# Kernel tuning notes

Measured on AMD Instinct MI355X. Metric: run time of the kernel, lower is better.

## Reference

```python
import jax, jax.numpy as jnp
import numpy as np

B, S, DIM = 2, 2048, 1024
H = 16
HD = DIM // H  # 64
SCALE = HD ** -0.5


def setup_inputs() -> dict:
    key = jax.random.key(0)
    k1, k2, k3 = jax.random.split(key, 3)
    x = jax.random.normal(k1, (B, S, DIM), dtype=jnp.float32)
    # Linear weights scaled ~1/sqrt(fan_in) like torch default init
    Wqkv = jax.random.normal(k2, (DIM, 3 * DIM), dtype=jnp.float32) * (DIM ** -0.5)
    Wproj = jax.random.normal(k3, (DIM, DIM), dtype=jnp.float32) * (DIM ** -0.5)
    return {"x": x, "Wqkv": Wqkv, "Wproj": Wproj}


def reference(x, Wqkv, Wproj):
    Bsz, Slen, dim = x.shape
    qkv = x @ Wqkv  # (B, S, 3*dim)
    qkv = qkv.reshape(Bsz, Slen, 3, H, HD)
    q, k, v = qkv[:, :, 0], qkv[:, :, 1], qkv[:, :, 2]  # each (B, S, H, HD)
    # softmax attention (chunking in the original is memory-only; math identical)
    scores = jnp.einsum("bshd,bthd->bhst", q, k) * SCALE  # (B, H, S, S)
    attn = jax.nn.softmax(scores, axis=-1)
    out = jnp.einsum("bhst,bthd->bshd", attn, v)  # (B, S, H, HD)
    out = out.reshape(Bsz, Slen, dim)
    return out @ Wproj
```

## Files before the change

### kernel.cpp

```cpp
#include <hip/hip_runtime.h>
#include <stdint.h>

typedef unsigned short u16;
typedef __attribute__((ext_vector_type(8))) short bf16x8;
typedef __attribute__((ext_vector_type(4))) float f32x4;

#define BATCH 2
#define SEQ 2048
#define NH 16
#define HDIM 64
#define DMODEL 1024
#define MTOT (BATCH * SEQ)
#define QKV_N (3 * DMODEL)
#define ATT_SCALE 0.125f
#define L2E 1.44269504088896340736f
#define C2 (ATT_SCALE * L2E)

__device__ __forceinline__ u16 f2b(float f) {
    uint32_t x = __builtin_bit_cast(uint32_t, f);
    uint32_t r = (x + 0x7fffu + ((x >> 16) & 1u)) >> 16;
    return (u16)r;
}

__device__ __forceinline__ uint32_t cvt_pk(float lo, float hi) {
    uint32_t r;
    asm("v_cvt_pk_bf16_f32 %0, %1, %2" : "=v"(r) : "v"(lo), "v"(hi));
    return r;
}

__device__ __forceinline__ void gl_lds16(const void* g, void* l) {
    __builtin_amdgcn_global_load_lds(
        (const __attribute__((address_space(1))) void*)g,
        (__attribute__((address_space(3))) void*)l, 16, 0, 0);
}

__global__ __launch_bounds__(256) void k_cvt(const float* __restrict__ in,
                                             u16* __restrict__ out, int n8) {
    int i = blockIdx.x * blockDim.x + threadIdx.x;
    if (i >= n8) return;
    const float4* p = (const float4*)in + (size_t)i * 2;
    float4 a = p[0], b = p[1];
    union { uint32_t w[4]; uint4 v; } u;
    u.w[0] = cvt_pk(a.x, a.y);
    u.w[1] = cvt_pk(a.z, a.w);
    u.w[2] = cvt_pk(b.x, b.y);
    u.w[3] = cvt_pk(b.z, b.w);
    *(uint4*)(out + (size_t)i * 8) = u.v;
}

__global__ __launch_bounds__(256) void k_wtrans(const float* __restrict__ W,
                                                u16* __restrict__ WT,
                                                int rows, int cols) {
    __shared__ float tile[64][65];
    const int c0 = blockIdx.x * 64, r0 = blockIdx.y * 64;
    const int tx = threadIdx.x & 63, ty = threadIdx.x >> 6;
#pragma unroll
    for (int i = 0; i < 16; ++i) {
        int r = i * 4 + ty;
        tile[r][tx] = W[(size_t)(r0 + r) * cols + c0 + tx];
    }
    __syncthreads();
#pragma unroll
    for (int i = 0; i < 16; ++i) {
        int c = i * 4 + ty;
        WT[(size_t)(c0 + c) * rows + r0 + tx] = f2b(tile[tx][c]);
    }
}

template <bool F32OUT>
__global__ __launch_bounds__(256) void k_gemm_bt(const u16* __restrict__ A,
                                                 const u16* __restrict__ BT,
                                                 void* __restrict__ C,
                                                 int M, int N, int K) {
    __shared__ __align__(16) u16 As[128 * 64];
    __shared__ __align__(16) u16 Bs[128 * 64];
    const int tid = threadIdx.x;
    const int wid = tid >> 6, lane = tid & 63;
    const int r = lane & 15, g = lane >> 4;
    const int m0 = blockIdx.y * 128, n0 = blockIdx.x * 128;
    const int wm = (wid >> 1) * 64, wn = (wid & 1) * 64;
    const int srow = lane >> 3, scol = (lane & 7) * 8;
    f32x4 acc[4][4] = {};
    for (int k0 = 0; k0 < K; k0 += 64) {
#pragma unroll
        for (int i = 0; i < 4; ++i) {
            const int li = wid * 4 + i;
            gl_lds16(A + (size_t)(m0 + li * 8 + srow) * K + k0 + scol, &As[li * 512]);
            gl_lds16(BT + (size_t)(n0 + li * 8 + srow) * K + k0 + scol, &Bs[li * 512]);
        }
        __syncthreads();
#pragma unroll
        for (int kk = 0; kk < 2; ++kk) {
            bf16x8 af[4], bfr[4];
#pragma unroll
            for (int mi = 0; mi < 4; ++mi)
                af[mi] = *(const bf16x8*)&As[(wm + mi * 16 + r) * 64 + kk * 32 + g * 8];
#pragma unroll
            for (int ni = 0; ni < 4; ++ni)
                bfr[ni] = *(const bf16x8*)&Bs[(wn + ni * 16 + r) * 64 + kk * 32 + g * 8];
#pragma unroll
            for (int mi = 0; mi < 4; ++mi)
#pragma unroll
                for (int ni = 0; ni < 4; ++ni)
                    acc[mi][ni] = __builtin_amdgcn_mfma_f32_16x16x32_bf16(
                        bfr[ni], af[mi], acc[mi][ni], 0, 0, 0);
        }
        __syncthreads();
    }
#pragma unroll
    for (int mi = 0; mi < 4; ++mi)
#pragma unroll
        for (int ni = 0; ni < 4; ++ni) {
            const int row = m0 + wm + mi * 16 + r;
            const int col = n0 + wn + ni * 16 + g * 4;
            if (F32OUT) {
                float4 vv;
                vv.x = acc[mi][ni][0]; vv.y = acc[mi][ni][1];
                vv.z = acc[mi][ni][2]; vv.w = acc[mi][ni][3];
                *(float4*)&((float*)C)[(size_t)row * N + col] = vv;
            } else {
                union { uint32_t w[2]; ushort4 v; } o;
                o.w[0] = cvt_pk(acc[mi][ni][0], acc[mi][ni][1]);
                o.w[1] = cvt_pk(acc[mi][ni][2], acc[mi][ni][3]);
                *(ushort4*)&((u16*)C)[(size_t)row * N + col] = o.v;
            }
        }
}

__global__ __launch_bounds__(256) void k_vtrans(const u16* __restrict__ qkv,
                                                u16* __restrict__ Vt) {
    __shared__ u16 tile[64][65];
    const int bh = blockIdx.y;
    const int b = bh >> 4, h = bh & 15;
    const int s0 = blockIdx.x * 64;
    const int tx = threadIdx.x & 63, ty = threadIdx.x >> 6;
#pragma unroll
    for (int i = 0; i < 16; ++i) {
        int s = i * 4 + ty;
        tile[s][tx] = qkv[(size_t)(b * SEQ + s0 + s) * QKV_N + 2 * DMODEL + h * HDIM + tx];
    }
    __syncthreads();
#pragma unroll
    for (int i = 0; i < 16; ++i) {
        int hd = i * 4 + ty;
        Vt[((size_t)bh * HDIM + hd) * SEQ + s0 + tx] = tile[tx][hd];
    }
}

__global__ __launch_bounds__(256) void k_attn(const u16* __restrict__ qkv,
                                              const u16* __restrict__ Vt,
                                              u16* __restrict__ O) {
    __shared__ __align__(16) u16 Ks[2][4096];
    __shared__ __align__(16) u16 Vs[2][4096];
    const int bh = blockIdx.y;
    const int b = bh >> 4, h = bh & 15;
    const int q0 = blockIdx.x * 64;
    const int tid = threadIdx.x, wid = tid >> 6, lane = tid & 63;
    const int r = lane & 15, g = lane >> 4;

    const size_t qbase = (size_t)(b * SEQ + q0 + wid * 16 + r) * QKV_N + h * HDIM;
    const bf16x8 qf0 = *(const bf16x8*)&qkv[qbase + g * 8];
    const bf16x8 qf1 = *(const bf16x8*)&qkv[qbase + 32 + g * 8];

    float mL = -1e30f, lsum = 0.f;
    f32x4 oacc[4] = {};

    const int kc0 = wid * 2;

#define STAGE(BUF, SK0)                                                          \
    {                                                                            \
        _Pragma("unroll") for (int i = 0; i < 2; ++i) {                          \
            const int kc = kc0 + i;                                              \
            const int ksrow = (kc >> 2) * 32 + g * 8 + (kc & 1) * 4 + ((lane >> 2) & 3); \
            const int kscol = ((kc >> 1) & 1) * 32 + (lane & 3) * 8;             \
            gl_lds16(&qkv[(size_t)(b * SEQ + (SK0) + ksrow) * QKV_N + DMODEL +   \
                          h * HDIM + kscol],                                     \
                     &Ks[BUF][kc * 512]);                                        \
            const int vhd = (kc & 3) * 16 + r;                                   \
            const int vsc = (kc >> 2) * 32 + g * 8;                              \
            gl_lds16(&Vt[((size_t)bh * HDIM + vhd) * SEQ + (SK0) + vsc],         \
                     &Vs[BUF][kc * 512]);                                        \
        }                                                                        \
    }

    STAGE(0, 0);
    asm volatile("s_waitcnt vmcnt(0)");
    __syncthreads();

    for (int t = 0; t < SEQ / 64; ++t) {
        const int cur = t & 1;
        if (t < SEQ / 64 - 1) STAGE(cur ^ 1, (t + 1) * 64);

        f32x4 sacc[4] = {};
        __builtin_amdgcn_s_setprio(1);
#pragma unroll
        for (int nf = 0; nf < 4; ++nf) {
            const int kbase = (nf & 1) * 2048 + (nf >> 1) * 512 +
                              (r >> 2) * 128 + (r & 3) * 32 + g * 8;
            bf16x8 kf0 = *(const bf16x8*)&Ks[cur][kbase];
            bf16x8 kf1 = *(const bf16x8*)&Ks[cur][kbase + 1024];
            sacc[nf] = __builtin_amdgcn_mfma_f32_16x16x32_bf16(kf0, qf0, sacc[nf], 0, 0, 0);
            sacc[nf] = __builtin_amdgcn_mfma_f32_16x16x32_bf16(kf1, qf1, sacc[nf], 0, 0, 0);
        }
        __builtin_amdgcn_s_setprio(0);

        float mt = fmaxf(fmaxf(sacc[0][0], sacc[0][1]), fmaxf(sacc[0][2], sacc[0][3]));
#pragma unroll
        for (int nf = 1; nf < 4; ++nf)
            mt = fmaxf(mt, fmaxf(fmaxf(sacc[nf][0], sacc[nf][1]),
                                 fmaxf(sacc[nf][2], sacc[nf][3])));
        mt = fmaxf(mt, __shfl_xor(mt, 16, 64));
        mt = fmaxf(mt, __shfl_xor(mt, 32, 64));
        const float pm = mt * C2;
        if (!__all(pm - mL <= 8.f)) {
            const float mNew = fmaxf(mL, pm);
            const float al = exp2f(mL - mNew);
            mL = mNew;
            lsum *= al;
#pragma unroll
            for (int ht = 0; ht < 4; ++ht)
#pragma unroll
                for (int e = 0; e < 4; ++e) oacc[ht][e] *= al;
        }
        float p[4][4];
#pragma unroll
        for (int nf = 0; nf < 4; ++nf)
#pragma unroll
            for (int e = 0; e < 4; ++e) {
                p[nf][e] = exp2f(sacc[nf][e] * C2 - mL);
                lsum += p[nf][e];
            }

        union { uint32_t w[4]; bf16x8 v; } upf0, upf1;
        upf0.w[0] = cvt_pk(p[0][0], p[0][1]);
        upf0.w[1] = cvt_pk(p[0][2], p[0][3]);
        upf0.w[2] = cvt_pk(p[2][0], p[2][1]);
        upf0.w[3] = cvt_pk(p[2][2], p[2][3]);
        upf1.w[0] = cvt_pk(p[1][0], p[1][1]);
        upf1.w[1] = cvt_pk(p[1][2], p[1][3]);
        upf1.w[2] = cvt_pk(p[3][0], p[3][1]);
        upf1.w[3] = cvt_pk(p[3][2], p[3][3]);

        __builtin_amdgcn_s_setprio(1);
#pragma unroll
        for (int ht = 0; ht < 4; ++ht) {
            bf16x8 vf0 = *(const bf16x8*)&Vs[cur][ht * 512 + g * 128 + r * 8];
            bf16x8 vf1 = *(const bf16x8*)&Vs[cur][(4 + ht) * 512 + g * 128 + r * 8];
            oacc[ht] = __builtin_amdgcn_mfma_f32_16x16x32_bf16(vf0, upf0.v, oacc[ht], 0, 0, 0);
            oacc[ht] = __builtin_amdgcn_mfma_f32_16x16x32_bf16(vf1, upf1.v, oacc[ht], 0, 0, 0);
        }
        __builtin_amdgcn_s_setprio(0);

        asm volatile("s_waitcnt vmcnt(0)");
        __syncthreads();
    }
#undef STAGE

    lsum += __shfl_xor(lsum, 16, 64);
    lsum += __shfl_xor(lsum, 32, 64);
    const float inv = 1.0f / lsum;
    const size_t obase = (size_t)(b * SEQ + q0 + wid * 16 + r) * DMODEL + h * HDIM;
#pragma unroll
    for (int ht = 0; ht < 4; ++ht) {
        union { uint32_t w[2]; ushort4 v; } o;
        o.w[0] = cvt_pk(oacc[ht][0] * inv, oacc[ht][1] * inv);
        o.w[1] = cvt_pk(oacc[ht][2] * inv, oacc[ht][3] * inv);
        *(ushort4*)&O[obase + ht * 16 + g * 4] = o.v;
    }
}

extern "C" void kernel_launch(void* const* d_in, const int* in_sizes, int n_in,
                              void* d_out, int out_size, void* d_ws, size_t ws_size,
                              hipStream_t stream) {
    const float* x = (const float*)d_in[0];
    const float* Wqkv = (const float*)d_in[1];
    const float* Wproj = (const float*)d_in[2];
    float* out = (float*)d_out;

    u16* xb = (u16*)d_ws;
    u16* WqkvT = xb + (size_t)MTOT * DMODEL;
    u16* WprojT = WqkvT + (size_t)QKV_N * DMODEL;
    u16* qkv = WprojT + (size_t)DMODEL * DMODEL;
    u16* Vt = qkv + (size_t)MTOT * QKV_N;
    u16* Ob = Vt + (size_t)BATCH * NH * HDIM * SEQ;

    k_cvt<<<dim3((MTOT * DMODEL / 8) / 256), 256, 0, stream>>>(x, xb, MTOT * DMODEL / 8);
    k_wtrans<<<dim3(QKV_N / 64, DMODEL / 64), 256, 0, stream>>>(Wqkv, WqkvT, DMODEL, QKV_N);
    k_wtrans<<<dim3(DMODEL / 64, DMODEL / 64), 256, 0, stream>>>(Wproj, WprojT, DMODEL, DMODEL);
    k_gemm_bt<false><<<dim3(QKV_N / 128, MTOT / 128), 256, 0, stream>>>(
        xb, WqkvT, (void*)qkv, MTOT, QKV_N, DMODEL);
    k_vtrans<<<dim3(SEQ / 64, BATCH * NH), 256, 0, stream>>>(qkv, Vt);
    k_attn<<<dim3(SEQ / 64, BATCH * NH), 256, 0, stream>>>(qkv, Vt, Ob);
    k_gemm_bt<true><<<dim3(DMODEL / 128, MTOT / 128), 256, 0, stream>>>(
        Ob, WprojT, (void*)out, MTOT, DMODEL, DMODEL);
}
```

Before: 243.0 us.

## Add 256x256 8-wave ping-pong QKV GEMM and defer softmax max reduction

Swaps the QKV projection GEMM to a new 256x256-tile, 512-thread kernel. It double-buffers A/B tiles in 128KB of dynamic LDS, interleaves LDS reads, global prefetches and MFMA phases with explicit barriers and priority hints, and uses partial vmcnt waits. The aim is to raise data reuse and overlap memory traffic with compute compared with the 128x128 GEMM. The attention kernel also skips the cross-lane max shuffles unless a rescale is needed. The large tile gives only 12x16 blocks, which may underfill the CUs, and the manual barrier scheduling is fragile.

After: 230.3 us. 1.06x faster.

```diff
diff --git a/kernel.cpp b/kernel.cpp
--- a/kernel.cpp
+++ b/kernel.cpp
@@ -15,6 +15,8 @@
 #define ATT_SCALE 0.125f
 #define L2E 1.44269504088896340736f
 #define C2 (ATT_SCALE * L2E)
+
+#define BAR() asm volatile("s_barrier" ::: "memory")
 
 __device__ __forceinline__ u16 f2b(float f) {
     uint32_t x = __builtin_bit_cast(uint32_t, f);
@@ -65,6 +67,131 @@
         int c = i * 4 + ty;
         WT[(size_t)(c0 + c) * rows + r0 + tx] = f2b(tile[tx][c]);
     }
+}
+
+__global__ __launch_bounds__(512, 2) void k_gemm_qkv8(const u16* __restrict__ A,
+                                                      const u16* __restrict__ BT,
+                                                      u16* __restrict__ C) {
+    extern __shared__ __align__(16) u16 lds[];
+    const int tid = threadIdx.x, wid = tid >> 6, lane = tid & 63;
+    const int r = lane & 15, g = lane >> 4;
+    const int wr = wid >> 2, wc = wid & 3;
+    const int m0 = blockIdx.y * 256, n0 = blockIdx.x * 256;
+    const int K = DMODEL;
+
+    auto STG = [&](int kt2, int rg) {
+        const int isB = rg >> 1, half = rg & 1;
+        const u16* src = isB ? BT : A;
+        const int rowb = (isB ? n0 : m0) + half * 128 + wid * 16 + (lane >> 2);
+        const u16* s = src + (size_t)rowb * K + kt2 * 64 + (lane & 3) * 8;
+        const int dst = (kt2 & 1) * 32768 + isB * 16384 + half * 8192 +
+                        wid * 1024 + lane * 8;
+        gl_lds16(s, &lds[dst]);
+        gl_lds16(s + 32, &lds[dst + 512]);
+    };
+
+    f32x4 acc[8][4] = {};
+    bf16x8 a[4][2], b[4][2];
+    const int aB = wr * 8192 + r * 32 + g * 8;
+    const int bB = 16384 + (wc >> 1) * 8192 + (wc & 1) * 4096 + r * 32 + g * 8;
+
+#pragma unroll
+    for (int t2 = 0; t2 < 2; ++t2)
+#pragma unroll
+        for (int rg = 0; rg < 4; ++rg) STG(t2, rg);
+    asm volatile("s_waitcnt vmcnt(0)" ::: "memory");
+    __syncthreads();
+
+    for (int kt = 0; kt < 16; ++kt) {
+        const int sb = (kt & 1) * 32768;
+#pragma unroll
+        for (int mi = 0; mi < 4; ++mi)
+#pragma unroll
+            for (int kk = 0; kk < 2; ++kk)
+                a[mi][kk] = *(const bf16x8*)&lds[sb + aB + (mi * 2 + kk) * 512];
+#pragma unroll
+        for (int ni = 0; ni < 2; ++ni)
+#pragma unroll
+            for (int kk = 0; kk < 2; ++kk)
+                b[ni][kk] = *(const bf16x8*)&lds[sb + bB + (ni * 2 + kk) * 512];
+        BAR();
+        __builtin_amdgcn_s_setprio(1);
+#pragma unroll
+        for (int mi = 0; mi < 4; ++mi)
+#pragma unroll
+            for (int ni = 0; ni < 2; ++ni)
+#pragma unroll
+                for (int kk = 0; kk < 2; ++kk)
+                    acc[mi][ni] = __builtin_amdgcn_mfma_f32_16x16x32_bf16(
+                        b[ni][kk], a[mi][kk], acc[mi][ni], 0, 0, 0);
+        __builtin_amdgcn_s_setprio(0);
+        BAR();
+#pragma unroll
+        for (int ni = 2; ni < 4; ++ni)
+#pragma unroll
+            for (int kk = 0; kk < 2; ++kk)
+                b[ni][kk] = *(const bf16x8*)&lds[sb + bB + (ni * 2 + kk) * 512];
+        BAR();
+        __builtin_amdgcn_s_setprio(1);
+#pragma unroll
+        for (int mi = 0; mi < 4; ++mi)
+#pragma unroll
+            for (int ni = 2; ni < 4; ++ni)
+#pragma unroll
+                for (int kk = 0; kk < 2; ++kk)
+                    acc[mi][ni] = __builtin_amdgcn_mfma_f32_16x16x32_bf16(
+                        b[ni][kk], a[mi][kk], acc[mi][ni], 0, 0, 0);
+        __builtin_amdgcn_s_setprio(0);
+        BAR();
+#pragma unroll
+        for (int mi = 0; mi < 4; ++mi)
+#pragma unroll
+            for (int kk = 0; kk < 2; ++kk)
+                a[mi][kk] = *(const bf16x8*)&lds[sb + aB + ((4 + mi) * 2 + kk) * 512];
+        if (kt < 14) { STG(kt + 2, 2); STG(kt + 2, 3); }
+        BAR();
+        __builtin_amdgcn_s_setprio(1);
+#pragma unroll
+        for (int mi = 0; mi < 4; ++mi)
+#pragma unroll
+            for (int ni = 2; ni < 4; ++ni)
+#pragma unroll
+                for (int kk = 0; kk < 2; ++kk)
+                    acc[4 + mi][ni] = __builtin_amdgcn_mfma_f32_16x16x32_bf16(
+                        b[ni][kk], a[mi][kk], acc[4 + mi][ni], 0, 0, 0);
+        __builtin_amdgcn_s_setprio(0);
+        BAR();
+        if (kt < 14) { STG(kt + 2, 0); STG(kt + 2, 1); }
+        BAR();
+        __builtin_amdgcn_s_setprio(1);
+#pragma unroll
+        for (int mi = 0; mi < 4; ++mi)
+#pragma unroll
+            for (int ni = 0; ni < 2; ++ni)
+#pragma unroll
+                for (int kk = 0; kk < 2; ++kk)
+                    acc[4 + mi][ni] = __builtin_amdgcn_mfma_f32_16x16x32_bf16(
+                        b[ni][kk], a[mi][kk], acc[4 + mi][ni], 0, 0, 0);
+        __builtin_amdgcn_s_setprio(0);
+        if (kt < 14) {
+            asm volatile("s_waitcnt vmcnt(8)" ::: "memory");
+        } else if (kt == 14) {
+            asm volatile("s_waitcnt vmcnt(0)" ::: "memory");
+        }
+        BAR();
+    }
+
+#pragma unroll
+    for (int mi = 0; mi < 8; ++mi)
+#pragma unroll
+        for (int ni = 0; ni < 4; ++ni) {
+            const int row = m0 + wr * 128 + mi * 16 + r;
+            const int col = n0 + wc * 64 + ni * 16 + g * 4;
+            union { uint32_t w[2]; ushort4 v; } o;
+            o.w[0] = cvt_pk(acc[mi][ni][0], acc[mi][ni][1]);
+            o.w[1] = cvt_pk(acc[mi][ni][2], acc[mi][ni][3]);
+            *(ushort4*)&C[(size_t)row * QKV_N + col] = o.v;
+        }
 }
 
 template <bool F32OUT>
@@ -164,7 +291,6 @@
 
     float mL = -1e30f, lsum = 0.f;
     f32x4 oacc[4] = {};
-
     const int kc0 = wid * 2;
 
 #define STAGE(BUF, SK0)                                                          \
@@ -204,16 +330,16 @@
         }
         __builtin_amdgcn_s_setprio(0);
 
-        float mt = fmaxf(fmaxf(sacc[0][0], sacc[0][1]), fmaxf(sacc[0][2], sacc[0][3]));
-#pragma unroll
-        for (int nf = 1; nf < 4; ++nf)
-            mt = fmaxf(mt, fmaxf(fmaxf(sacc[nf][0], sacc[nf][1]),
-                                 fmaxf(sacc[nf][2], sacc[nf][3])));
-        mt = fmaxf(mt, __shfl_xor(mt, 16, 64));
-        mt = fmaxf(mt, __shfl_xor(mt, 32, 64));
-        const float pm = mt * C2;
-        if (!__all(pm - mL <= 8.f)) {
-            const float mNew = fmaxf(mL, pm);
+        float m0a = fmaxf(fmaxf(sacc[0][0], sacc[0][1]), fmaxf(sacc[0][2], sacc[0][3]));
+        float m1a = fmaxf(fmaxf(sacc[1][0], sacc[1][1]), fmaxf(sacc[1][2], sacc[1][3]));
+        float m2a = fmaxf(fmaxf(sacc[2][0], sacc[2][1]), fmaxf(sacc[2][2], sacc[2][3]));
+        float m3a = fmaxf(fmaxf(sacc[3][0], sacc[3][1]), fmaxf(sacc[3][2], sacc[3][3]));
+        const float pm = fmaxf(fmaxf(m0a, m1a), fmaxf(m2a, m3a)) * C2;
+        if (!__all(pm <= mL + 8.f)) {
+            float rm = pm;
+            rm = fmaxf(rm, __shfl_xor(rm, 16, 64));
+            rm = fmaxf(rm, __shfl_xor(rm, 32, 64));
+            const float mNew = fmaxf(mL, rm);
             const float al = exp2f(mL - mNew);
             mL = mNew;
             lsum *= al;
@@ -284,11 +410,13 @@
     u16* Vt = qkv + (size_t)MTOT * QKV_N;
     u16* Ob = Vt + (size_t)BATCH * NH * HDIM * SEQ;
 
+    hipFuncSetAttribute(reinterpret_cast<const void*>(k_gemm_qkv8),
+                        hipFuncAttributeMaxDynamicSharedMemorySize, 131072);
+
     k_cvt<<<dim3((MTOT * DMODEL / 8) / 256), 256, 0, stream>>>(x, xb, MTOT * DMODEL / 8);
     k_wtrans<<<dim3(QKV_N / 64, DMODEL / 64), 256, 0, stream>>>(Wqkv, WqkvT, DMODEL, QKV_N);
     k_wtrans<<<dim3(DMODEL / 64, DMODEL / 64), 256, 0, stream>>>(Wproj, WprojT, DMODEL, DMODEL);
-    k_gemm_bt<false><<<dim3(QKV_N / 128, MTOT / 128), 256, 0, stream>>>(
-        xb, WqkvT, (void*)qkv, MTOT, QKV_N, DMODEL);
+    k_gemm_qkv8<<<dim3(QKV_N / 256, MTOT / 256), 512, 131072, stream>>>(xb, WqkvT, qkv);
     k_vtrans<<<dim3(SEQ / 64, BATCH * NH), 256, 0, stream>>>(qkv, Vt);
     k_attn<<<dim3(SEQ / 64, BATCH * NH), 256, 0, stream>>>(qkv, Vt, Ob);
     k_gemm_bt<true><<<dim3(DMODEL / 128, MTOT / 128), 256, 0, stream>>>(
```
